# Performance work log

Measured on AMD Instinct MI355X. Metric: run time of the kernel, lower is better.

The kernel has to match this reference:

```python
import jax, jax.numpy as jnp
import numpy as np

D_K = 64

def setup_inputs() -> dict:
    key = jax.random.key(0)
    ks = jax.random.split(key, 9)
    B, S, D = 8, 2048, 512
    d_k, d_v = 64, 64
    return {
        "q_in": jax.random.normal(ks[0], (B, S, D), jnp.float32),
        "k_in": jax.random.normal(ks[1], (B, S, D), jnp.float32),
        "v_in": jax.random.normal(ks[2], (B, S, D), jnp.float32),
        "Wq": jax.random.normal(ks[3], (D, d_k), jnp.float32) * 0.05,
        "bq": jax.random.normal(ks[4], (d_k,), jnp.float32) * 0.05,
        "Wk": jax.random.normal(ks[5], (D, d_k), jnp.float32) * 0.05,
        "bk": jax.random.normal(ks[6], (d_k,), jnp.float32) * 0.05,
        "Wv": jax.random.normal(ks[7], (D, d_v), jnp.float32) * 0.05,
        "bv": jax.random.normal(ks[8], (d_v,), jnp.float32) * 0.05,
    }

def reference(q_in, k_in, v_in, Wq, bq, Wk, bk, Wv, bv):
    # Dense projections: x @ W + b
    q = jnp.einsum('bsd,dk->bsk', q_in, Wq) + bq  # [B,S,d_k]
    k = jnp.einsum('bsd,dk->bsk', k_in, Wk) + bk  # [B,S,d_k]
    v = jnp.einsum('bsd,dv->bsv', v_in, Wv) + bv  # [B,S,d_v]
    scale = 1.0 / np.sqrt(D_K).astype(np.float32)
    scores = jnp.einsum('bqk,bsk->bqs', q, k) * scale  # [B,S,S]
    attn = jax.nn.softmax(scores, axis=-1)
    return jnp.einsum('bqs,bsv->bqv', attn, v)  # [B,S,d_v]
```

## Files before the change

### kernel.cpp

```cpp
#include <hip/hip_runtime.h>
#include <hip/hip_bf16.h>
#include <cstdint>

typedef __attribute__((ext_vector_type(8))) short short8;
typedef __attribute__((ext_vector_type(16))) float f32x16;

#if __has_builtin(__builtin_amdgcn_exp2f)
#define EXP2F(x) __builtin_amdgcn_exp2f(x)
#else
#define EXP2F(x) exp2f(x)
#endif

#define MFMA32(A, B, C) __builtin_amdgcn_mfma_f32_32x32x16_bf16((A), (B), (C), 0, 0, 0)

__device__ __forceinline__ unsigned short f2bf(float f) {
  unsigned int u = __builtin_bit_cast(unsigned int, f);
  u += 0x7FFFu + ((u >> 16) & 1u);
  return (unsigned short)(u >> 16);
}

__global__ __launch_bounds__(256) void prep_wt(
    const float* __restrict__ Wq, const float* __restrict__ Wk,
    const float* __restrict__ Wv, unsigned short* __restrict__ Wt)
{
  int idx = blockIdx.x * 256 + threadIdx.x;
  int which = idx >> 15;
  int rem = idx & 32767;
  int n = rem >> 9;
  int k = rem & 511;
  const float* W = (which == 0) ? Wq : (which == 1) ? Wk : Wv;
  Wt[idx] = f2bf(W[k * 64 + n]);
}

__global__ __launch_bounds__(256, 3) void proj_kernel(
    const float* __restrict__ qin, const float* __restrict__ kin,
    const float* __restrict__ vin, const unsigned short* __restrict__ Wt,
    const float* __restrict__ bq, const float* __restrict__ bk,
    const float* __restrict__ bv,
    unsigned short* __restrict__ Qo, unsigned short* __restrict__ Ko,
    unsigned short* __restrict__ Vto)
{
  __shared__ unsigned short Xs[2][64 * 136];

  const int which = blockIdx.y;
  const float* X    = (which == 0) ? qin : (which == 1) ? kin : vin;
  const float* bias = (which == 0) ? bq  : (which == 1) ? bk  : bv;

  const int tid = threadIdx.x;
  const int lane = tid & 63, wv = tid >> 6;
  const int h = lane >> 5, l31 = lane & 31;
  const int grp = wv & 1, nh = wv >> 1;
  const int m0 = blockIdx.x * 64;

  const unsigned short* wcol =
      Wt + (size_t)which * 64 * 512 + (size_t)(nh * 32 + l31) * 512 + h * 8;

  const int srow = tid >> 5;
  const int skoff = tid & 31;
  const float* xg = X + (size_t)(m0 + srow) * 512 + skoff * 4;

  #pragma unroll
  for (int j = 0; j < 8; ++j) {
    float4 a = *(const float4*)(xg + (size_t)(8 * j) * 512);
    unsigned int w0 = (unsigned int)f2bf(a.x) | ((unsigned int)f2bf(a.y) << 16);
    unsigned int w1 = (unsigned int)f2bf(a.z) | ((unsigned int)f2bf(a.w) << 16);
    uint2 pw; pw.x = w0; pw.y = w1;
    *(uint2*)(&Xs[0][(srow + 8 * j) * 136 + skoff * 4]) = pw;
  }
  __syncthreads();

  f32x16 acc = {};
  for (int c = 0; c < 4; ++c) {
    float4 pf[8];
    if (c < 3) {
      #pragma unroll
      for (int j = 0; j < 8; ++j)
        pf[j] = *(const float4*)(xg + (size_t)(8 * j) * 512 + (c + 1) * 128);
    }
    const unsigned short* arow = &Xs[c & 1][(grp * 32 + l31) * 136 + h * 8];
    const unsigned short* wk = wcol + c * 128;
    #pragma unroll
    for (int ks = 0; ks < 8; ++ks) {
      short8 af = *(const short8*)(arow + ks * 16);
      short8 bf = *(const short8*)(wk + ks * 16);
      acc = MFMA32(af, bf, acc);
    }
    if (c < 3) {
      unsigned short* dst = Xs[(c + 1) & 1];
      #pragma unroll
      for (int j = 0; j < 8; ++j) {
        unsigned int w0 = (unsigned int)f2bf(pf[j].x) | ((unsigned int)f2bf(pf[j].y) << 16);
        unsigned int w1 = (unsigned int)f2bf(pf[j].z) | ((unsigned int)f2bf(pf[j].w) << 16);
        uint2 pw; pw.x = w0; pw.y = w1;
        *(uint2*)(&dst[(srow + 8 * j) * 136 + skoff * 4]) = pw;
      }
      __syncthreads();
    }
  }

  const float bv0 = bias[nh * 32 + l31];

  if (which < 2) {
    const float scale = which ? 1.0f : 0.18033688f;
    unsigned short* Y = which ? Ko : Qo;
    #pragma unroll
    for (int r = 0; r < 16; ++r) {
      int row = (r & 3) + 8 * (r >> 2) + 4 * h;
      Y[(size_t)(m0 + grp * 32 + row) * 64 + nh * 32 + l31] =
          f2bf((acc[r] + bv0) * scale);
    }
  } else {
    __syncthreads();
    unsigned short* TB = Xs[0];
    #pragma unroll
    for (int r = 0; r < 16; ++r) {
      int row = (r & 3) + 8 * (r >> 2) + 4 * h;
      TB[(nh * 32 + l31) * 68 + grp * 32 + row] = f2bf(acc[r] + bv0);
    }
    __syncthreads();
    int bidx = blockIdx.x >> 5;
    int s0 = (blockIdx.x & 31) * 64;
    for (int i = tid; i < 64 * 16; i += 256) {
      int n = i >> 4, cs = i & 15;
      ushort4 v4 = *(const ushort4*)(TB + n * 68 + cs * 4);
      *(ushort4*)(Vto + ((size_t)bidx * 64 + n) * 2048 + s0 + cs * 4) = v4;
    }
  }
}

__global__ __launch_bounds__(512, 2) void attn_kernel(
    const unsigned short* __restrict__ Q, const unsigned short* __restrict__ K,
    const unsigned short* __restrict__ Vt, float* __restrict__ out)
{
  __shared__ float ObS[4][16][64];
  __shared__ float MpS[4][64];
  __shared__ float LpS[4][64];

  const int tid = threadIdx.x;
  const int lane = tid & 63, w = tid >> 6;
  const int h = lane >> 5, l31 = lane & 31;
  const int b = blockIdx.x & 7;
  const int q0 = (blockIdx.x >> 3) * 64;

  short8 qf[2][4];
  #pragma unroll
  for (int qt = 0; qt < 2; ++qt) {
    const unsigned short* qp = Q + ((size_t)(b * 2048 + q0 + qt * 32 + l31)) * 64 + h * 8;
    #pragma unroll
    for (int c = 0; c < 4; ++c) qf[qt][c] = *(const short8*)(qp + c * 16);
  }

  f32x16 o00 = {}, o01 = {}, o10 = {}, o11 = {};
  float m0 = -1e30f, m1 = -1e30f, ls0 = 0.f, ls1 = 0.f;

  for (int st = 0; st < 8; ++st) {
    const int kb = w * 256 + st * 32;
    short8 kf[4];
    const unsigned short* kp = K + ((size_t)(b * 2048 + kb + l31)) * 64 + h * 8;
    #pragma unroll
    for (int c = 0; c < 4; ++c) kf[c] = *(const short8*)(kp + c * 16);
    short8 vf0[2], vf1[2];
    {
      const unsigned short* vp0 = Vt + ((size_t)(b * 64 + l31)) * 2048 + kb + h * 8;
      const unsigned short* vp1 = Vt + ((size_t)(b * 64 + 32 + l31)) * 2048 + kb + h * 8;
      vf0[0] = *(const short8*)(vp0);  vf0[1] = *(const short8*)(vp0 + 16);
      vf1[0] = *(const short8*)(vp1);  vf1[1] = *(const short8*)(vp1 + 16);
    }
    #pragma unroll
    for (int qt = 0; qt < 2; ++qt) {
      f32x16 sT = {};
      #pragma unroll
      for (int c = 0; c < 4; ++c) sT = MFMA32(kf[c], qf[qt][c], sT);
      float mx = sT[0];
      #pragma unroll
      for (int r = 1; r < 16; ++r) mx = fmaxf(mx, sT[r]);
      mx = fmaxf(mx, __shfl_xor(mx, 32, 64));
      float mold = qt ? m1 : m0;
      float mnew = fmaxf(mold, mx);
      float alpha = EXP2F(mold - mnew);
      float rs = 0.f;
      float p[16];
      #pragma unroll
      for (int r = 0; r < 16; ++r) { p[r] = EXP2F(sT[r] - mnew); rs += p[r]; }
      rs += __shfl_xor(rs, 32, 64);
      unsigned int pk[8];
      #pragma unroll
      for (int i = 0; i < 8; ++i)
        pk[i] = (unsigned int)f2bf(p[2 * i]) | ((unsigned int)f2bf(p[2 * i + 1]) << 16);
      unsigned int ex[8];
      #pragma unroll
      for (int i = 0; i < 8; ++i) ex[i] = (unsigned int)__shfl_xor((int)pk[i], 32, 64);
      uint4 cc0, cc1;
      if (h == 0) { cc0 = make_uint4(pk[0], pk[1], ex[0], ex[1]); cc1 = make_uint4(pk[4], pk[5], ex[4], ex[5]); }
      else        { cc0 = make_uint4(ex[2], ex[3], pk[2], pk[3]); cc1 = make_uint4(ex[6], ex[7], pk[6], pk[7]); }
      short8 P0 = __builtin_bit_cast(short8, cc0);
      short8 P1 = __builtin_bit_cast(short8, cc1);
      if (qt == 0) {
        m0 = mnew; ls0 = ls0 * alpha + rs;
        o00 *= alpha; o10 *= alpha;
        o00 = MFMA32(vf0[0], P0, o00); o00 = MFMA32(vf0[1], P1, o00);
        o10 = MFMA32(vf1[0], P0, o10); o10 = MFMA32(vf1[1], P1, o10);
      } else {
        m1 = mnew; ls1 = ls1 * alpha + rs;
        o01 *= alpha; o11 *= alpha;
        o01 = MFMA32(vf0[0], P0, o01); o01 = MFMA32(vf0[1], P1, o01);
        o11 = MFMA32(vf1[0], P0, o11); o11 = MFMA32(vf1[1], P1, o11);
      }
    }
  }

  for (int half = 4; half > 0; half >>= 1) {
    const bool writer = (w >= half) && (w < 2 * half);
    const bool merger = (w < half);
    __syncthreads();
    if (writer && h == 0) {
      MpS[w - half][l31] = m0;      LpS[w - half][l31] = ls0;
      MpS[w - half][32 + l31] = m1; LpS[w - half][32 + l31] = ls1;
    }
    __syncthreads();
    float fb0 = 0.f, fb1 = 0.f;
    if (merger) {
      float pm0 = MpS[w][l31],      pl0 = LpS[w][l31];
      float pm1 = MpS[w][32 + l31], pl1 = LpS[w][32 + l31];
      float nm0 = fmaxf(m0, pm0), nm1 = fmaxf(m1, pm1);
      float fa0 = EXP2F(m0 - nm0); fb0 = EXP2F(pm0 - nm0);
      float fa1 = EXP2F(m1 - nm1); fb1 = EXP2F(pm1 - nm1);
      m0 = nm0; m1 = nm1;
      ls0 = ls0 * fa0 + pl0 * fb0; ls1 = ls1 * fa1 + pl1 * fb1;
      o00 *= fa0; o10 *= fa0; o01 *= fa1; o11 *= fa1;
    }
    __syncthreads();
    if (writer) {
      #pragma unroll
      for (int r = 0; r < 16; ++r) ObS[w - half][r][lane] = o00[r]; }
    __syncthreads();
    if (merger) {
      #pragma unroll
      for (int r = 0; r < 16; ++r) o00[r] += ObS[w][r][lane] * fb0; }
    __syncthreads();
    if (writer) {
      #pragma unroll
      for (int r = 0; r < 16; ++r) ObS[w - half][r][lane] = o01[r]; }
    __syncthreads();
    if (merger) {
      #pragma unroll
      for (int r = 0; r < 16; ++r) o01[r] += ObS[w][r][lane] * fb1; }
    __syncthreads();
    if (writer) {
      #pragma unroll
      for (int r = 0; r < 16; ++r) ObS[w - half][r][lane] = o10[r]; }
    __syncthreads();
    if (merger) {
      #pragma unroll
      for (int r = 0; r < 16; ++r) o10[r] += ObS[w][r][lane] * fb0; }
    __syncthreads();
    if (writer) {
      #pragma unroll
      for (int r = 0; r < 16; ++r) ObS[w - half][r][lane] = o11[r]; }
    __syncthreads();
    if (merger) {
      #pragma unroll
      for (int r = 0; r < 16; ++r) o11[r] += ObS[w][r][lane] * fb1; }
  }

  if (w == 0) {
    float i0 = 1.0f / ls0, i1 = 1.0f / ls1;
    o00 *= i0; o10 *= i0; o01 *= i1; o11 *= i1;
    #pragma unroll
    for (int qt = 0; qt < 2; ++qt) {
      int q = qt * 32 + l31;
      float* ob = out + ((size_t)(b * 2048 + q0 + q)) * 64 + 4 * h;
      const f32x16 a = qt ? o01 : o00;
      const f32x16 c = qt ? o11 : o10;
      #pragma unroll
      for (int g = 0; g < 4; ++g) {
        *(float4*)(ob + 8 * g)      = make_float4(a[4*g], a[4*g+1], a[4*g+2], a[4*g+3]);
        *(float4*)(ob + 32 + 8 * g) = make_float4(c[4*g], c[4*g+1], c[4*g+2], c[4*g+3]);
      }
    }
  }
}

extern "C" void kernel_launch(void* const* d_in, const int* in_sizes, int n_in,
                              void* d_out, int out_size, void* d_ws, size_t ws_size,
                              hipStream_t stream) {
  const float* qin = (const float*)d_in[0];
  const float* kin = (const float*)d_in[1];
  const float* vin = (const float*)d_in[2];
  const float* Wq  = (const float*)d_in[3];
  const float* bq  = (const float*)d_in[4];
  const float* Wk  = (const float*)d_in[5];
  const float* bk  = (const float*)d_in[6];
  const float* Wv  = (const float*)d_in[7];
  const float* bv  = (const float*)d_in[8];

  unsigned short* Qo  = (unsigned short*)d_ws;
  unsigned short* Ko  = Qo + (size_t)16384 * 64;
  unsigned short* Vto = Ko + (size_t)16384 * 64;
  unsigned short* Wt  = Vto + (size_t)8 * 64 * 2048;
  float* out = (float*)d_out;

  hipLaunchKernelGGL(prep_wt, dim3(384), dim3(256), 0, stream, Wq, Wk, Wv, Wt);
  hipLaunchKernelGGL(proj_kernel, dim3(256, 3), dim3(256), 0, stream,
                     qin, kin, vin, Wt, bq, bk, bv, Qo, Ko, Vto);
  hipLaunchKernelGGL(attn_kernel, dim3(256), dim3(512), 0, stream, Qo, Ko, Vto, out);
}
```

Before: 162.5 us.

## Replace tree reduction of per-wave softmax partials with single-pass LDS merge

The cross-wave merge of flash-attention partial outputs previously ran three rounds of pairwise merges, each with many __syncthreads and serialized LDS round trips. It now computes the global max and denominator for each query row in one step from shared stats. Each wave pre-scales its accumulators, and waves 4-7 are folded into waves 0-3 through one large LDS buffer. The final sum and output store are then spread across all 8 waves. This cuts barrier count and gives every wave work in the epilogue, at the cost of a larger shared-memory footprint (64KB), which could limit two-blocks-per-CU occupancy.

```diff
diff --git a/kernel.cpp b/kernel.cpp
--- a/kernel.cpp
+++ b/kernel.cpp
@@ -132,9 +132,9 @@
     const unsigned short* __restrict__ Q, const unsigned short* __restrict__ K,
     const unsigned short* __restrict__ Vt, float* __restrict__ out)
 {
-  __shared__ float ObS[4][16][64];
-  __shared__ float MpS[4][64];
-  __shared__ float LpS[4][64];
+  __shared__ float Obuf[4][16][4][64];
+  float* Mex = &Obuf[0][0][0][0];
+  float* Lex = Mex + 512;
 
   const int tid = threadIdx.x;
   const int lane = tid & 63, w = tid >> 6;
@@ -209,75 +209,72 @@
     }
   }
 
-  for (int half = 4; half > 0; half >>= 1) {
-    const bool writer = (w >= half) && (w < 2 * half);
-    const bool merger = (w < half);
-    __syncthreads();
-    if (writer && h == 0) {
-      MpS[w - half][l31] = m0;      LpS[w - half][l31] = ls0;
-      MpS[w - half][32 + l31] = m1; LpS[w - half][32 + l31] = ls1;
-    }
-    __syncthreads();
-    float fb0 = 0.f, fb1 = 0.f;
-    if (merger) {
-      float pm0 = MpS[w][l31],      pl0 = LpS[w][l31];
-      float pm1 = MpS[w][32 + l31], pl1 = LpS[w][32 + l31];
-      float nm0 = fmaxf(m0, pm0), nm1 = fmaxf(m1, pm1);
-      float fa0 = EXP2F(m0 - nm0); fb0 = EXP2F(pm0 - nm0);
-      float fa1 = EXP2F(m1 - nm1); fb1 = EXP2F(pm1 - nm1);
-      m0 = nm0; m1 = nm1;
-      ls0 = ls0 * fa0 + pl0 * fb0; ls1 = ls1 * fa1 + pl1 * fb1;
-      o00 *= fa0; o10 *= fa0; o01 *= fa1; o11 *= fa1;
-    }
-    __syncthreads();
-    if (writer) {
-      #pragma unroll
-      for (int r = 0; r < 16; ++r) ObS[w - half][r][lane] = o00[r]; }
-    __syncthreads();
-    if (merger) {
-      #pragma unroll
-      for (int r = 0; r < 16; ++r) o00[r] += ObS[w][r][lane] * fb0; }
-    __syncthreads();
-    if (writer) {
-      #pragma unroll
-      for (int r = 0; r < 16; ++r) ObS[w - half][r][lane] = o01[r]; }
-    __syncthreads();
-    if (merger) {
-      #pragma unroll
-      for (int r = 0; r < 16; ++r) o01[r] += ObS[w][r][lane] * fb1; }
-    __syncthreads();
-    if (writer) {
-      #pragma unroll
-      for (int r = 0; r < 16; ++r) ObS[w - half][r][lane] = o10[r]; }
-    __syncthreads();
-    if (merger) {
-      #pragma unroll
-      for (int r = 0; r < 16; ++r) o10[r] += ObS[w][r][lane] * fb0; }
-    __syncthreads();
-    if (writer) {
-      #pragma unroll
-      for (int r = 0; r < 16; ++r) ObS[w - half][r][lane] = o11[r]; }
-    __syncthreads();
-    if (merger) {
-      #pragma unroll
-      for (int r = 0; r < 16; ++r) o11[r] += ObS[w][r][lane] * fb1; }
-  }
-
-  if (w == 0) {
-    float i0 = 1.0f / ls0, i1 = 1.0f / ls1;
-    o00 *= i0; o10 *= i0; o01 *= i1; o11 *= i1;
-    #pragma unroll
-    for (int qt = 0; qt < 2; ++qt) {
-      int q = qt * 32 + l31;
-      float* ob = out + ((size_t)(b * 2048 + q0 + q)) * 64 + 4 * h;
-      const f32x16 a = qt ? o01 : o00;
-      const f32x16 c = qt ? o11 : o10;
-      #pragma unroll
-      for (int g = 0; g < 4; ++g) {
-        *(float4*)(ob + 8 * g)      = make_float4(a[4*g], a[4*g+1], a[4*g+2], a[4*g+3]);
-        *(float4*)(ob + 32 + 8 * g) = make_float4(c[4*g], c[4*g+1], c[4*g+2], c[4*g+3]);
-      }
-    }
+  if (h == 0) {
+    Mex[w * 64 + l31]      = m0;  Mex[w * 64 + 32 + l31] = m1;
+    Lex[w * 64 + l31]      = ls0; Lex[w * 64 + 32 + l31] = ls1;
+  }
+  __syncthreads();
+  float M0 = -1e30f, M1 = -1e30f;
+  #pragma unroll
+  for (int w2 = 0; w2 < 8; ++w2) {
+    M0 = fmaxf(M0, Mex[w2 * 64 + l31]);
+    M1 = fmaxf(M1, Mex[w2 * 64 + 32 + l31]);
+  }
+  float L0 = 0.f, L1 = 0.f;
+  #pragma unroll
+  for (int w2 = 0; w2 < 8; ++w2) {
+    L0 += Lex[w2 * 64 + l31] * EXP2F(Mex[w2 * 64 + l31] - M0);
+    L1 += Lex[w2 * 64 + 32 + l31] * EXP2F(Mex[w2 * 64 + 32 + l31] - M1);
+  }
+  float fac0 = EXP2F(m0 - M0) / L0;
+  float fac1 = EXP2F(m1 - M1) / L1;
+  __syncthreads();
+
+  o00 *= fac0; o10 *= fac0; o01 *= fac1; o11 *= fac1;
+
+  if (w >= 4) {
+    #pragma unroll
+    for (int r = 0; r < 16; ++r) {
+      Obuf[0][r][w - 4][lane] = o00[r];
+      Obuf[1][r][w - 4][lane] = o01[r];
+      Obuf[2][r][w - 4][lane] = o10[r];
+      Obuf[3][r][w - 4][lane] = o11[r];
+    }
+  }
+  __syncthreads();
+  if (w < 4) {
+    #pragma unroll
+    for (int r = 0; r < 16; ++r) {
+      o00[r] += Obuf[0][r][w][lane];
+      o01[r] += Obuf[1][r][w][lane];
+      o10[r] += Obuf[2][r][w][lane];
+      o11[r] += Obuf[3][r][w][lane];
+    }
+    #pragma unroll
+    for (int r = 0; r < 16; ++r) {
+      Obuf[0][r][w][lane] = o00[r];
+      Obuf[1][r][w][lane] = o01[r];
+      Obuf[2][r][w][lane] = o10[r];
+      Obuf[3][r][w][lane] = o11[r];
+    }
+  }
+  __syncthreads();
+
+  #pragma unroll
+  for (int ui = 0; ui < 2; ++ui) {
+    int u = 2 * w + ui;
+    int f = u >> 2, g = u & 3;
+    int qt = f & 1, vt = f >> 1;
+    float val[4];
+    #pragma unroll
+    for (int j = 0; j < 4; ++j) {
+      int r = 4 * g + j;
+      val[j] = Obuf[f][r][0][lane] + Obuf[f][r][1][lane]
+             + Obuf[f][r][2][lane] + Obuf[f][r][3][lane];
+    }
+    int q = qt * 32 + l31;
+    float* ob = out + ((size_t)(b * 2048 + q0 + q)) * 64 + vt * 32 + 8 * g + 4 * h;
+    *(float4*)ob = make_float4(val[0], val[1], val[2], val[3]);
   }
 }
 
```

Result: no change. 162.6 us (+0.0%).
